# Kernel optimization log

Measured on AMD Instinct MI355X. Metric: run time of the kernel, lower is better.

The kernel has to match this reference:

```python
import jax, jax.numpy as jnp
import numpy as np

B, LV, LT, D, TD, H = 64, 1024, 128, 256, 1536, 4
HD = D // H
KEEP_RATIO = 0.5
K = min(max(int(np.ceil(LV * KEEP_RATIO)), 1), LV)
ND = LV - K  # number of dropped tokens
EPS_NORM = 1e-12


def setup_inputs() -> dict:
    key = jax.random.key(0)
    ks = jax.random.split(key, 9)
    s = 0.02
    return {
        "hidden_v": jax.random.normal(ks[0], (B, LV, D), jnp.float32),
        "hidden_t": jax.random.normal(ks[1], (B, LT, TD), jnp.float32),
        "senti_t": jax.random.normal(ks[2], (B, LT), jnp.float32),
        "mask_v": jnp.ones((B, LV), dtype=bool),
        "mask_t": jnp.ones((B, LT), dtype=bool),
        "W_t": jax.random.normal(ks[3], (D, TD), jnp.float32) * s,
        "b_t": jnp.zeros((D,), jnp.float32),
        "Wq": jax.random.normal(ks[4], (D, D), jnp.float32) * s,
        "bq": jnp.zeros((D,), jnp.float32),
        "Wk": jax.random.normal(ks[5], (D, D), jnp.float32) * s,
        "bk": jnp.zeros((D,), jnp.float32),
    }


def _l2norm(x):
    n = jnp.linalg.norm(x, axis=-1, keepdims=True)
    return x / jnp.maximum(n, EPS_NORM)


def _prune_one(V_b, score_b):
    """V_b: [LV, D], score_b: [LV] -> (V_merge [K, D], top_idx [K])."""
    _, top_idx = jax.lax.top_k(score_b, K)
    top_idx = jnp.sort(top_idx)
    V_keep = V_b[top_idx]                       # [K, D]
    drop_mask = jnp.ones((LV,), bool).at[top_idx].set(False)
    ar = jnp.arange(LV)
    drop_idx = jnp.sort(jnp.where(drop_mask, ar, LV + ar))[:ND]  # [ND], sorted
    V_drop = V_b[drop_idx]                      # [ND, D]
    score_drop = score_b[drop_idx]              # [ND]
    # bipartite cosine-similarity assignment of dropped -> kept
    sim = _l2norm(V_drop) @ _l2norm(V_keep).T   # [ND, K]
    assign = jnp.argmax(sim, axis=1)            # [ND]
    # per-cluster softmax over dropped-token scores (segment softmax)
    seg_max = jax.ops.segment_max(score_drop, assign, num_segments=K)
    w = jnp.exp(score_drop - seg_max[assign])
    denom = jax.ops.segment_sum(w, assign, num_segments=K)
    w = w / jnp.maximum(denom[assign], EPS_NORM)
    merged = jax.ops.segment_sum(w[:, None] * V_drop, assign, num_segments=K)
    has_member = jax.ops.segment_sum(jnp.ones((ND,), V_b.dtype), assign, num_segments=K) > 0
    V_merge = _l2norm(V_keep + merged)
    V_out = jnp.where(has_member[:, None], V_merge, V_keep)
    return V_out, top_idx


def reference(hidden_v, hidden_t, senti_t, mask_v, mask_t, W_t, b_t, Wq, bq, Wk, bk):
    mt = mask_t.astype(jnp.float32)
    # text projection + sentiment weights
    T = hidden_t @ W_t.T + b_t                                   # [B, LT, D]
    w_t = jnp.abs(senti_t) * mt
    w_t = w_t / (w_t.sum(axis=1, keepdims=True) + 1e-8)
    w_t = w_t * mt
    # cross-attention weights (averaged over heads); attn_out is unused by the module
    q = (hidden_v @ Wq.T + bq).reshape(B, LV, H, HD)
    k = (T @ Wk.T + bk).reshape(B, LT, H, HD)
    scores = jnp.einsum('bqhd,bkhd->bhqk', q, k) / np.sqrt(HD)   # [B, H, LV, LT]
    scores = jnp.where(mask_t[:, None, None, :], scores, -1e9)
    attn = jax.nn.softmax(scores, axis=-1).mean(axis=1)          # [B, LV, LT]
    score_v = jnp.einsum('bqk,bk->bq', attn, w_t)                # [B, LV]
    score_v = jnp.where(mask_v, score_v, -1e9)
    hidden_v_new, retained_indices = jax.vmap(_prune_one)(hidden_v, score_v)
    return hidden_v_new, retained_indices
```

## Files before the change

### kernel.cpp

```cpp
#include <hip/hip_runtime.h>
#include <math.h>

#define B_ 64
#define LV_ 1024
#define LT_ 128
#define D_ 256
#define TD_ 1536
#define H_ 4
#define HD_ 64
#define K_ 512
#define ND_ 512

__device__ float g_M[TD_ * D_];
__device__ float g_WqT[D_ * D_];
__device__ float g_WkT[D_ * D_];
__device__ float g_kbias[D_];
__device__ float g_wt[B_ * LT_];
__device__ float g_KmatT[(size_t)B_ * D_ * LT_];
__device__ float g_Q[(size_t)B_ * LV_ * D_];
__device__ float g_score[B_ * LV_];
__device__ int   g_tidx[B_ * K_];
__device__ int   g_didx[B_ * ND_];
__device__ float g_sdrop[B_ * ND_];
__device__ int   g_assign[B_ * ND_];
__device__ float g_kninv[B_ * K_];


__device__ __forceinline__ float f4c(const float4& v, int i) {
  return ((const float*)&v)[i];
}

__global__ __launch_bounds__(256) void prep1_kernel(
    const float* __restrict__ Wk, const float* __restrict__ Wq,
    const float* __restrict__ bt, const float* __restrict__ bk) {
  int bx = blockIdx.x, t = threadIdx.x;
  if (bx < D_) {
    g_WkT[bx * D_ + t] = Wk[t * D_ + bx];
  } else if (bx < 2 * D_) {
    int j = bx - D_;
    g_WqT[j * D_ + t] = Wq[t * D_ + j];
  } else {
    float acc = bk[t];
    for (int e = 0; e < D_; ++e) acc += bt[e] * Wk[t * D_ + e];
    g_kbias[t] = acc;
  }
}

__global__ __launch_bounds__(256) void prep2_kernel(const float* __restrict__ Wt) {
  int j0 = blockIdx.x * 16;
  int t = threadIdx.x;
  __shared__ float WtL[256 * 20];
  const float4* Wt4 = (const float4*)Wt;
#pragma unroll
  for (int i = 0; i < 4; ++i) {
    int idx = i * 256 + t;
    int e = idx >> 2, j4 = idx & 3;
    float4 v = Wt4[e * (TD_ / 4) + (j0 >> 2) + j4];
    WtL[e * 20 + 4 * j4 + 0] = v.x;
    WtL[e * 20 + 4 * j4 + 1] = v.y;
    WtL[e * 20 + 4 * j4 + 2] = v.z;
    WtL[e * 20 + 4 * j4 + 3] = v.w;
  }
  __syncthreads();
  float acc[16];
#pragma unroll
  for (int jj = 0; jj < 16; ++jj) acc[jj] = 0.f;
  for (int e = 0; e < D_; ++e) {
    float wk = g_WkT[e * D_ + t];
#pragma unroll
    for (int q4 = 0; q4 < 4; ++q4) {
      float4 w = *(const float4*)&WtL[e * 20 + 4 * q4];
      acc[4 * q4 + 0] += w.x * wk;
      acc[4 * q4 + 1] += w.y * wk;
      acc[4 * q4 + 2] += w.z * wk;
      acc[4 * q4 + 3] += w.w * wk;
    }
  }
#pragma unroll
  for (int jj = 0; jj < 16; ++jj) g_M[(j0 + jj) * D_ + t] = acc[jj];
}

__global__ __launch_bounds__(128) void wt_kernel(const float* __restrict__ senti) {
  int b = blockIdx.x, t = threadIdx.x;
  __shared__ float red[128];
  float v = fabsf(senti[b * LT_ + t]);
  red[t] = v;
  __syncthreads();
  for (int s = 64; s > 0; s >>= 1) {
    if (t < s) red[t] += red[t + s];
    __syncthreads();
  }
  g_wt[b * LT_ + t] = v / (red[0] + 1e-8f);
}

__global__ __launch_bounds__(256) void kproj_kernel(const float* __restrict__ ht) {
  int b = blockIdx.x >> 3;
  int l0 = (blockIdx.x & 7) * 16;
  int t = threadIdx.x;
  __shared__ float htT[256 * 20];
  int lq = t >> 6;
  int dq = t & 63;
  float acc[4][4];
#pragma unroll
  for (int li = 0; li < 4; ++li)
#pragma unroll
    for (int di = 0; di < 4; ++di) acc[li][di] = 0.f;
  const float4* M4 = (const float4*)g_M;
  const float4* ht4 = (const float4*)ht;
  for (int e0 = 0; e0 < TD_; e0 += 256) {
    __syncthreads();
#pragma unroll
    for (int i = 0; i < 4; ++i) {
      int idx = i * 256 + t;
      int e4 = idx >> 4, l = idx & 15;
      float4 v = ht4[(size_t)(b * LT_ + l0 + l) * (TD_ / 4) + (e0 >> 2) + e4];
      htT[(4 * e4 + 0) * 20 + l] = v.x;
      htT[(4 * e4 + 1) * 20 + l] = v.y;
      htT[(4 * e4 + 2) * 20 + l] = v.z;
      htT[(4 * e4 + 3) * 20 + l] = v.w;
    }
    __syncthreads();
    for (int e = 0; e < 256; ++e) {
      float4 m = M4[(size_t)(e0 + e) * 64 + dq];
      float4 hl = *(const float4*)&htT[e * 20 + 4 * lq];
#pragma unroll
      for (int li = 0; li < 4; ++li) {
        float hs = f4c(hl, li);
        acc[li][0] += hs * m.x;
        acc[li][1] += hs * m.y;
        acc[li][2] += hs * m.z;
        acc[li][3] += hs * m.w;
      }
    }
  }
  float4 kb = *(const float4*)(g_kbias + 4 * dq);
  __syncthreads();
#pragma unroll
  for (int li = 0; li < 4; ++li) {
    float o0 = acc[li][0] + kb.x;
    float o1 = acc[li][1] + kb.y;
    float o2 = acc[li][2] + kb.z;
    float o3 = acc[li][3] + kb.w;
    int l = 4 * lq + li;
    htT[(4 * dq + 0) * 17 + l] = o0;
    htT[(4 * dq + 1) * 17 + l] = o1;
    htT[(4 * dq + 2) * 17 + l] = o2;
    htT[(4 * dq + 3) * 17 + l] = o3;
  }
  __syncthreads();
#pragma unroll
  for (int i = 0; i < 16; ++i) {
    int idx = i * 256 + t;
    int l = idx & 15, d = idx >> 4;
    g_KmatT[((size_t)b * D_ + d) * LT_ + l0 + l] = htT[d * 17 + l];
  }
}

__global__ __launch_bounds__(256, 4) void qproj_kernel(
    const float* __restrict__ hv, const float* __restrict__ bq) {
  int b = blockIdx.y;
  int q0 = blockIdx.x * 32;
  int t = threadIdx.x;
  int co = t & 31;
  int rq = t >> 5;
  float acc[4][8];
#pragma unroll
  for (int c = 0; c < 8; ++c) {
    float bqv = bq[8 * co + c];
#pragma unroll
    for (int ri = 0; ri < 4; ++ri) acc[ri][c] = bqv;
  }
  const float4* hv4 = (const float4*)(hv + ((size_t)b * LV_ + q0) * D_);
  for (int j4 = 0; j4 < 64; ++j4) {
    float4 hq[4];
#pragma unroll
    for (int ri = 0; ri < 4; ++ri) hq[ri] = hv4[(4 * rq + ri) * 64 + j4];
#pragma unroll
    for (int jj = 0; jj < 4; ++jj) {
      const float4* w4 = (const float4*)(g_WqT + (4 * j4 + jj) * D_ + 8 * co);
      float4 wa = w4[0], wb = w4[1];
#pragma unroll
      for (int ri = 0; ri < 4; ++ri) {
        float hvv = f4c(hq[ri], jj);
        acc[ri][0] += hvv * wa.x;
        acc[ri][1] += hvv * wa.y;
        acc[ri][2] += hvv * wa.z;
        acc[ri][3] += hvv * wa.w;
        acc[ri][4] += hvv * wb.x;
        acc[ri][5] += hvv * wb.y;
        acc[ri][6] += hvv * wb.z;
        acc[ri][7] += hvv * wb.w;
      }
    }
  }
  float4* gQ4 = (float4*)(g_Q + ((size_t)b * LV_ + q0) * D_);
#pragma unroll
  for (int ri = 0; ri < 4; ++ri) {
    gQ4[(4 * rq + ri) * 64 + 2 * co + 0] =
        make_float4(acc[ri][0], acc[ri][1], acc[ri][2], acc[ri][3]);
    gQ4[(4 * rq + ri) * 64 + 2 * co + 1] =
        make_float4(acc[ri][4], acc[ri][5], acc[ri][6], acc[ri][7]);
  }
}

__global__ __launch_bounds__(256, 4) void score2_kernel() {
  int b = blockIdx.y;
  int q0 = blockIdx.x * 32;
  int t = threadIdx.x;
  __shared__ float kT[32 * 128];
  int kq = t & 31;
  int qq = t >> 5;
  float4 wtv = ((const float4*)(g_wt + b * LT_))[kq];
  float svacc[4] = {0.f, 0.f, 0.f, 0.f};
  const float4* kmt4 = (const float4*)(g_KmatT + (size_t)b * D_ * LT_);
  const float4* gQ4 = (const float4*)(g_Q + ((size_t)b * LV_ + q0) * D_);
  float4* kT4w = (float4*)kT;
  const float4* kT4 = (const float4*)kT;
  float4 pre[4];
#pragma unroll
  for (int i = 0; i < 4; ++i) {
    int idx = i * 256 + t;
    pre[i] = kmt4[(idx >> 5) * 32 + (idx & 31)];
  }
  for (int h = 0; h < H_; ++h) {
    float sacc[4][4];
#pragma unroll
    for (int ri = 0; ri < 4; ++ri)
#pragma unroll
      for (int ki = 0; ki < 4; ++ki) sacc[ri][ki] = 0.f;
    for (int half = 0; half < 2; ++half) {
      if (h | half) __syncthreads();
#pragma unroll
      for (int i = 0; i < 4; ++i) kT4w[i * 256 + t] = pre[i];
      int s = h * 2 + half + 1;
      if (s < 8) {
        int hn = s >> 1, hf = s & 1;
#pragma unroll
        for (int i = 0; i < 4; ++i) {
          int idx = i * 256 + t;
          pre[i] = kmt4[(size_t)(hn * 64 + hf * 32 + (idx >> 5)) * 32 + (idx & 31)];
        }
      }
      __syncthreads();
#pragma unroll
      for (int d4l = 0; d4l < 8; ++d4l) {
        float4 qv[4], kv[4];
#pragma unroll
        for (int ri = 0; ri < 4; ++ri)
          qv[ri] = gQ4[(4 * qq + ri) * 64 + h * 16 + half * 8 + d4l];
#pragma unroll
        for (int dd = 0; dd < 4; ++dd)
          kv[dd] = kT4[(4 * d4l + dd) * 32 + kq];
#pragma unroll
        for (int dd = 0; dd < 4; ++dd)
#pragma unroll
          for (int ri = 0; ri < 4; ++ri) {
            float qs = f4c(qv[ri], dd);
            sacc[ri][0] += qs * kv[dd].x;
            sacc[ri][1] += qs * kv[dd].y;
            sacc[ri][2] += qs * kv[dd].z;
            sacc[ri][3] += qs * kv[dd].w;
          }
      }
    }
#pragma unroll
    for (int ri = 0; ri < 4; ++ri) {
      float s0 = sacc[ri][0] * 0.125f, s1 = sacc[ri][1] * 0.125f;
      float s2 = sacc[ri][2] * 0.125f, s3 = sacc[ri][3] * 0.125f;
      float m = fmaxf(fmaxf(s0, s1), fmaxf(s2, s3));
#pragma unroll
      for (int off = 16; off > 0; off >>= 1) m = fmaxf(m, __shfl_xor(m, off));
      float e0 = expf(s0 - m), e1 = expf(s1 - m);
      float e2 = expf(s2 - m), e3 = expf(s3 - m);
      float es = e0 + e1 + e2 + e3;
      float cs = e0 * wtv.x + e1 * wtv.y + e2 * wtv.z + e3 * wtv.w;
#pragma unroll
      for (int off = 16; off > 0; off >>= 1) {
        es += __shfl_xor(es, off);
        cs += __shfl_xor(cs, off);
      }
      svacc[ri] += cs / es;
    }
  }
  if (kq == 0) {
#pragma unroll
    for (int ri = 0; ri < 4; ++ri)
      g_score[(size_t)b * LV_ + q0 + 4 * qq + ri] = svacc[ri] * 0.25f;
  }
}

__global__ __launch_bounds__(1024) void topk_kernel(float* __restrict__ out_idx) {
  int b = blockIdx.x, t = threadIdx.x;
  __shared__ float s[LV_];
  __shared__ unsigned char keep[LV_];
  s[t] = g_score[(size_t)b * LV_ + t];
  __syncthreads();
  float mys = s[t];
  int cnt = 0;
  for (int jj = 0; jj < LV_; ++jj) {
    float sj = s[jj];
    cnt += (sj > mys || (sj == mys && jj < t)) ? 1 : 0;
  }
  int kp = (cnt < K_) ? 1 : 0;
  keep[t] = (unsigned char)kp;
  __syncthreads();
  int pos = 0;
  for (int jj = 0; jj < t; ++jj) pos += keep[jj];
  if (kp) {
    g_tidx[b * K_ + pos] = t;
    out_idx[b * K_ + pos] = (float)t;
  } else {
    int dp = t - pos;
    g_didx[b * ND_ + dp] = t;
    g_sdrop[b * ND_ + dp] = mys;
  }
}

__global__ __launch_bounds__(256) void knorm_kernel(const float* __restrict__ hv) {
  int b = blockIdx.y;
  int k = blockIdx.x * 256 + threadIdx.x;
  int src = g_tidx[b * K_ + k];
  const float4* row = (const float4*)(hv + ((size_t)b * LV_ + src) * D_);
  float acc = 0.f;
  for (int c = 0; c < 64; ++c) {
    float4 v = row[c];
    acc += v.x * v.x;
    acc += v.y * v.y;
    acc += v.z * v.z;
    acc += v.w * v.w;
  }
  g_kninv[b * K_ + k] = 1.f / fmaxf(sqrtf(acc), 1e-12f);
}

__global__ __launch_bounds__(256, 3) void assign_kernel(const float* __restrict__ hv) {
  int b = blockIdx.y;
  int n0 = blockIdx.x * 32;
  int t = threadIdx.x;
  __shared__ float smem[32 * 9 * 4 + 32 * 128];
  float* VdL = smem;
  float* VkT = smem + 1152;
  float* bestv = smem;
  int* bestk = (int*)(smem + 1024);

  int tn = t >> 5;
  int tk = t & 31;
  int rstage = t >> 3;
  int c8 = t & 7;

  int didx_t = g_didx[b * ND_ + n0 + rstage];
  const float4* vd_src = (const float4*)(hv + ((size_t)b * LV_ + didx_t) * D_);

  float bv[4] = {-INFINITY, -INFINITY, -INFINITY, -INFINITY};
  int bk[4] = {0, 0, 0, 0};

  for (int kt = 0; kt < 4; ++kt) {
    const float4* vk_src[4];
#pragma unroll
    for (int i = 0; i < 4; ++i) {
      int kl = i * 32 + rstage;
      int tix = g_tidx[b * K_ + kt * 128 + kl];
      vk_src[i] = (const float4*)(hv + ((size_t)b * LV_ + tix) * D_);
    }
    float4 kn4 = ((const float4*)(g_kninv + (size_t)b * K_ + kt * 128))[tk];
    float acc[4][4][4];
#pragma unroll
    for (int ri = 0; ri < 4; ++ri)
#pragma unroll
      for (int kj = 0; kj < 4; ++kj)
#pragma unroll
        for (int c = 0; c < 4; ++c) acc[ri][kj][c] = 0.f;
    for (int dc = 0; dc < 8; ++dc) {
      __syncthreads();
      {
        float4 v = vd_src[dc * 8 + c8];
        ((float4*)VdL)[rstage * 9 + c8] = v;
      }
#pragma unroll
      for (int i = 0; i < 4; ++i) {
        int kl = i * 32 + rstage;
        float4 v = vk_src[i][dc * 8 + c8];
        int col = ((((kl >> 2) ^ c8) << 2) | (kl & 3));
        VkT[(4 * c8 + 0) * 128 + col] = v.x;
        VkT[(4 * c8 + 1) * 128 + col] = v.y;
        VkT[(4 * c8 + 2) * 128 + col] = v.z;
        VkT[(4 * c8 + 3) * 128 + col] = v.w;
      }
      __syncthreads();
      const float4* VdL4 = (const float4*)VdL;
      const float4* VkT4 = (const float4*)VkT;
#pragma unroll
      for (int d4l = 0; d4l < 8; ++d4l) {
        float4 vd[4], kv[4];
#pragma unroll
        for (int ri = 0; ri < 4; ++ri)
          vd[ri] = VdL4[(4 * tn + ri) * 9 + d4l];
#pragma unroll
        for (int dd = 0; dd < 4; ++dd)
          kv[dd] = VkT4[(4 * d4l + dd) * 32 + (tk ^ d4l)];
#pragma unroll
        for (int dd = 0; dd < 4; ++dd)
#pragma unroll
          for (int ri = 0; ri < 4; ++ri) {
            float a = f4c(vd[ri], dd);
            acc[ri][0][dd] += a * kv[dd].x;
            acc[ri][1][dd] += a * kv[dd].y;
            acc[ri][2][dd] += a * kv[dd].z;
            acc[ri][3][dd] += a * kv[dd].w;
          }
      }
    }
#pragma unroll
    for (int ri = 0; ri < 4; ++ri) {
#pragma unroll
      for (int kj = 0; kj < 4; ++kj) {
        float s = (acc[ri][kj][0] + acc[ri][kj][1]) + (acc[ri][kj][2] + acc[ri][kj][3]);
        float v = s * f4c(kn4, kj);
        int kg = kt * 128 + 4 * tk + kj;
        if (v > bv[ri]) { bv[ri] = v; bk[ri] = kg; }
      }
    }
  }
  __syncthreads();
#pragma unroll
  for (int ri = 0; ri < 4; ++ri) {
    bestv[(4 * tn + ri) * 32 + tk] = bv[ri];
    bestk[(4 * tn + ri) * 32 + tk] = bk[ri];
  }
  __syncthreads();
  if (t < 32) {
    float bvf = bestv[t * 32];
    int bkf = bestk[t * 32];
    for (int q = 1; q < 32; ++q) {
      float v = bestv[t * 32 + q];
      int kx = bestk[t * 32 + q];
      if (v > bvf || (v == bvf && kx < bkf)) { bvf = v; bkf = kx; }
    }
    g_assign[b * ND_ + n0 + t] = bkf;
  }
}

__global__ __launch_bounds__(64) void merge_kernel(
    const float* __restrict__ hv, float* __restrict__ out_v) {
  int b = blockIdx.y, k = blockIdx.x;
  int lane = threadIdx.x;
  __shared__ int mem[ND_];
  int base = 0;
  for (int c = 0; c < ND_; c += 64) {
    int a = g_assign[b * ND_ + c + lane];
    unsigned long long msk = __ballot(a == k);
    if (a == k) {
      int pos = base + __popcll(msk & ((1ULL << lane) - 1ULL));
      mem[pos] = c + lane;
    }
    base += __popcll(msk);
  }
  __syncthreads();
  int src = g_tidx[b * K_ + k];
  float4 vk = ((const float4*)(hv + ((size_t)b * LV_ + src) * D_))[lane];
  float4 res;
  if (base > 0) {
    float mx = -INFINITY;
    for (int i = lane; i < base; i += 64) mx = fmaxf(mx, g_sdrop[b * ND_ + mem[i]]);
#pragma unroll
    for (int o = 32; o > 0; o >>= 1) mx = fmaxf(mx, __shfl_xor(mx, o));
    float dsum = 0.f;
    for (int i = lane; i < base; i += 64) dsum += expf(g_sdrop[b * ND_ + mem[i]] - mx);
#pragma unroll
    for (int o = 32; o > 0; o >>= 1) dsum += __shfl_xor(dsum, o);
    dsum = fmaxf(dsum, 1e-12f);
    float4 acc = {0.f, 0.f, 0.f, 0.f};
    for (int i = 0; i < base; ++i) {
      int n = mem[i];
      float w = expf(g_sdrop[b * ND_ + n] - mx) / dsum;
      float4 ud = ((const float4*)(hv + ((size_t)b * LV_ + g_didx[b * ND_ + n]) * D_))[lane];
      acc.x += w * ud.x; acc.y += w * ud.y;
      acc.z += w * ud.z; acc.w += w * ud.w;
    }
    float4 s4 = {vk.x + acc.x, vk.y + acc.y, vk.z + acc.z, vk.w + acc.w};
    float ss = s4.x * s4.x + s4.y * s4.y + s4.z * s4.z + s4.w * s4.w;
#pragma unroll
    for (int o = 32; o > 0; o >>= 1) ss += __shfl_xor(ss, o);
    float scale = 1.f / fmaxf(sqrtf(ss), 1e-12f);
    res.x = s4.x * scale; res.y = s4.y * scale; res.z = s4.z * scale; res.w = s4.w * scale;
  } else {
    res = vk;
  }
  ((float4*)(out_v + ((size_t)b * K_ + k) * D_))[lane] = res;
}

extern "C" void kernel_launch(void* const* d_in, const int* in_sizes, int n_in,
                              void* d_out, int out_size, void* d_ws, size_t ws_size,
                              hipStream_t stream) {
  const float* hv = (const float*)d_in[0];
  const float* ht = (const float*)d_in[1];
  const float* senti = (const float*)d_in[2];
  const float* Wt = (const float*)d_in[5];
  const float* bt = (const float*)d_in[6];
  const float* Wq = (const float*)d_in[7];
  const float* bq = (const float*)d_in[8];
  const float* Wk = (const float*)d_in[9];
  const float* bk = (const float*)d_in[10];
  (void)in_sizes; (void)n_in; (void)out_size; (void)d_ws; (void)ws_size;

  float* out_v = (float*)d_out;
  float* out_idx = out_v + (size_t)B_ * K_ * D_;

  hipLaunchKernelGGL(prep1_kernel, dim3(2 * D_ + 1), dim3(256), 0, stream, Wk, Wq, bt, bk);
  hipLaunchKernelGGL(prep2_kernel, dim3(TD_ / 16), dim3(256), 0, stream, Wt);
  hipLaunchKernelGGL(wt_kernel, dim3(B_), dim3(128), 0, stream, senti);
  hipLaunchKernelGGL(kproj_kernel, dim3(B_ * 8), dim3(256), 0, stream, ht);
  hipLaunchKernelGGL(qproj_kernel, dim3(LV_ / 32, B_), dim3(256), 0, stream, hv, bq);
  hipLaunchKernelGGL(score2_kernel, dim3(LV_ / 32, B_), dim3(256), 0, stream);
  hipLaunchKernelGGL(topk_kernel, dim3(B_), dim3(1024), 0, stream, out_idx);
  hipLaunchKernelGGL(knorm_kernel, dim3(2, B_), dim3(256), 0, stream, hv);
  hipLaunchKernelGGL(assign_kernel, dim3(ND_ / 32, B_), dim3(256), 0, stream, hv);
  hipLaunchKernelGGL(merge_kernel, dim3(K_, B_), dim3(64), 0, stream, hv, out_v);
}
```

Before: 904.2 us.

## Restructure Q projection to stage transposed hidden rows in shared memory

```diff
diff --git a/kernel.cpp b/kernel.cpp
--- a/kernel.cpp
+++ b/kernel.cpp
@@ -156,50 +156,50 @@
   }
 }
 
-__global__ __launch_bounds__(256, 4) void qproj_kernel(
+__global__ __launch_bounds__(256) void qproj_kernel(
     const float* __restrict__ hv, const float* __restrict__ bq) {
-  int b = blockIdx.y;
-  int q0 = blockIdx.x * 32;
+  int b = blockIdx.x >> 6;
+  int q0 = (blockIdx.x & 63) * 16;
   int t = threadIdx.x;
-  int co = t & 31;
-  int rq = t >> 5;
-  float acc[4][8];
-#pragma unroll
-  for (int c = 0; c < 8; ++c) {
-    float bqv = bq[8 * co + c];
-#pragma unroll
-    for (int ri = 0; ri < 4; ++ri) acc[ri][c] = bqv;
-  }
-  const float4* hv4 = (const float4*)(hv + ((size_t)b * LV_ + q0) * D_);
-  for (int j4 = 0; j4 < 64; ++j4) {
-    float4 hq[4];
-#pragma unroll
-    for (int ri = 0; ri < 4; ++ri) hq[ri] = hv4[(4 * rq + ri) * 64 + j4];
-#pragma unroll
-    for (int jj = 0; jj < 4; ++jj) {
-      const float4* w4 = (const float4*)(g_WqT + (4 * j4 + jj) * D_ + 8 * co);
-      float4 wa = w4[0], wb = w4[1];
-#pragma unroll
-      for (int ri = 0; ri < 4; ++ri) {
-        float hvv = f4c(hq[ri], jj);
-        acc[ri][0] += hvv * wa.x;
-        acc[ri][1] += hvv * wa.y;
-        acc[ri][2] += hvv * wa.z;
-        acc[ri][3] += hvv * wa.w;
-        acc[ri][4] += hvv * wb.x;
-        acc[ri][5] += hvv * wb.y;
-        acc[ri][6] += hvv * wb.z;
-        acc[ri][7] += hvv * wb.w;
-      }
-    }
-  }
-  float4* gQ4 = (float4*)(g_Q + ((size_t)b * LV_ + q0) * D_);
-#pragma unroll
-  for (int ri = 0; ri < 4; ++ri) {
-    gQ4[(4 * rq + ri) * 64 + 2 * co + 0] =
-        make_float4(acc[ri][0], acc[ri][1], acc[ri][2], acc[ri][3]);
-    gQ4[(4 * rq + ri) * 64 + 2 * co + 1] =
-        make_float4(acc[ri][4], acc[ri][5], acc[ri][6], acc[ri][7]);
+  __shared__ float hvT[256 * 20];
+  int lq = t >> 6;
+  int dq = t & 63;
+  const float4* hv4 = (const float4*)hv;
+#pragma unroll
+  for (int i = 0; i < 4; ++i) {
+    int idx = i * 256 + t;
+    int e4 = idx >> 4, l = idx & 15;
+    float4 v = hv4[(size_t)(b * LV_ + q0 + l) * 64 + e4];
+    hvT[(4 * e4 + 0) * 20 + l] = v.x;
+    hvT[(4 * e4 + 1) * 20 + l] = v.y;
+    hvT[(4 * e4 + 2) * 20 + l] = v.z;
+    hvT[(4 * e4 + 3) * 20 + l] = v.w;
+  }
+  float4 bqv = *(const float4*)(bq + 4 * dq);
+  float acc[4][4];
+#pragma unroll
+  for (int li = 0; li < 4; ++li)
+#pragma unroll
+    for (int di = 0; di < 4; ++di) acc[li][di] = f4c(bqv, di);
+  __syncthreads();
+  const float4* W4 = (const float4*)g_WqT;
+  for (int e = 0; e < 256; ++e) {
+    float4 w = W4[e * 64 + dq];
+    float4 hl = *(const float4*)&hvT[e * 20 + 4 * lq];
+#pragma unroll
+    for (int li = 0; li < 4; ++li) {
+      float hs = f4c(hl, li);
+      acc[li][0] += hs * w.x;
+      acc[li][1] += hs * w.y;
+      acc[li][2] += hs * w.z;
+      acc[li][3] += hs * w.w;
+    }
+  }
+  float4* gQ4 = (float4*)g_Q;
+#pragma unroll
+  for (int li = 0; li < 4; ++li) {
+    gQ4[(size_t)(b * LV_ + q0 + 4 * lq + li) * 64 + dq] =
+        make_float4(acc[li][0], acc[li][1], acc[li][2], acc[li][3]);
   }
 }
 
@@ -509,7 +509,7 @@
   hipLaunchKernelGGL(prep2_kernel, dim3(TD_ / 16), dim3(256), 0, stream, Wt);
   hipLaunchKernelGGL(wt_kernel, dim3(B_), dim3(128), 0, stream, senti);
   hipLaunchKernelGGL(kproj_kernel, dim3(B_ * 8), dim3(256), 0, stream, ht);
-  hipLaunchKernelGGL(qproj_kernel, dim3(LV_ / 32, B_), dim3(256), 0, stream, hv, bq);
+  hipLaunchKernelGGL(qproj_kernel, dim3(B_ * (LV_ / 16)), dim3(256), 0, stream, hv, bq);
   hipLaunchKernelGGL(score2_kernel, dim3(LV_ / 32, B_), dim3(256), 0, stream);
   hipLaunchKernelGGL(topk_kernel, dim3(B_), dim3(1024), 0, stream, out_idx);
   hipLaunchKernelGGL(knorm_kernel, dim3(2, B_), dim3(256), 0, stream, hv);
```

Result: faster. 864.9 us (-4.3%).
